# Optimization experiments

Hardware: AMD Instinct MI355X
Metric: run time of the kernel (lower is better)

Reference implementation:

```python
import jax, jax.numpy as jnp
import numpy as np

SCALE = 8.0  # (dim // n_heads) ** 0.5 = (1024 // 16) ** 0.5


def setup_inputs() -> dict:
    key = jax.random.key(0)
    kq, kk, kv = jax.random.split(key, 3)
    shape = (2, 16, 2048, 64)  # [B, H, N, Dh]
    q = jax.random.normal(kq, shape, dtype=jnp.float32)
    k = jax.random.normal(kk, shape, dtype=jnp.float32)
    v = jax.random.normal(kv, shape, dtype=jnp.float32)
    return {"q": q, "k": k, "v": v}


def reference(q, k, v):
    # scores[b,h,n,m] = sum_d q[b,h,n,d] * k[b,h,m,d], then MULTIPLIED by scale
    # (the original multiplies by sqrt(head_dim), it does not divide).
    scores = jnp.einsum('bhnd,bhmd->bhnm', q, k) * SCALE
    scores = jax.nn.softmax(scores, axis=-1)
    # Faithful to the original quirky einsum: sums over n (query axis), keeps m.
    # out[b,h,m,d] = (sum_n scores[b,h,n,m]) * v[b,h,m,d]
    out = jnp.einsum('bhnm,bhmd->bhmd', scores, v)
    return out
```

## Files before the change

### kernel.cpp

```cpp
#include <hip/hip_runtime.h>
#include <math.h>

#define BH 32
#define NN 2048
#define DD 64
#define BHNN (BH * NN)
#define QK ((size_t)BH * NN * DD)
#define LDK 72

#define QSCALE 11.5415603f

typedef __attribute__((ext_vector_type(8)))  _Float16 halfx8;
typedef __attribute__((ext_vector_type(4)))  _Float16 halfx4;
typedef __attribute__((ext_vector_type(16))) float    floatx16;

__device__ inline float fexp2(float x) { return __builtin_amdgcn_exp2f(x); }

__device__ inline int rowmap(int r, int half) {
    return (r & 3) + 8 * (r >> 2) + 4 * half;
}

__global__ __launch_bounds__(256) void convert_kernel(const float4* __restrict__ q,
                                                      const float4* __restrict__ k,
                                                      _Float16* __restrict__ qhi,
                                                      _Float16* __restrict__ qlo,
                                                      _Float16* __restrict__ khi) {
    size_t gid = (size_t)blockIdx.x * 256 + threadIdx.x;
    float4 qa = q[gid];
    float4 ka = k[gid];
    float qf[4] = {qa.x, qa.y, qa.z, qa.w};
    float kf[4] = {ka.x, ka.y, ka.z, ka.w};
    halfx4 h, l, kh;
#pragma unroll
    for (int i = 0; i < 4; ++i) {
        float f = qf[i] * QSCALE;
        _Float16 hh = (_Float16)f;
        h[i] = hh;
        l[i] = (_Float16)(f - (float)hh);
        kh[i] = (_Float16)kf[i];
    }
    *(halfx4*)&qhi[gid * 4] = h;
    *(halfx4*)&qlo[gid * 4] = l;
    *(halfx4*)&khi[gid * 4] = kh;
}

__device__ inline void load_tile(const _Float16* __restrict__ khi_t,
                                 int tid, halfx8 rh[4]) {
#pragma unroll
    for (int i = 0; i < 4; ++i) {
        int c = tid + 256 * i;
        int r = c >> 3, s = c & 7;
        rh[i] = *(const halfx8*)&khi_t[(size_t)r * 64 + s * 8];
    }
}
__device__ inline void write_tile(_Float16* Khi, int tid, const halfx8 rh[4]) {
#pragma unroll
    for (int i = 0; i < 4; ++i) {
        int c = tid + 256 * i;
        int r = c >> 3, s = c & 7;
        *(halfx8*)&Khi[r * LDK + s * 8] = rh[i];
    }
}

__device__ inline void load_a(const _Float16* __restrict__ qhi_row,
                              const _Float16* __restrict__ qlo_row,
                              int half, halfx8 ah[4], halfx8 al[4]) {
#pragma unroll
    for (int ks = 0; ks < 4; ++ks) {
        ah[ks] = *(const halfx8*)&qhi_row[ks * 16 + half * 8];
        al[ks] = *(const halfx8*)&qlo_row[ks * 16 + half * 8];
    }
}

__global__ __launch_bounds__(256, 3) void stats_kernel(const _Float16* __restrict__ qhi,
                                                       const _Float16* __restrict__ qlo,
                                                       const _Float16* __restrict__ khi,
                                                       float* __restrict__ smax_p,
                                                       float* __restrict__ sden_p) {
    __shared__ _Float16 Khi[128 * LDK];
    const int g    = blockIdx.x & 63;
    const int bh   = g & 31;
    const int ms   = g >> 5;
    const int n0   = (blockIdx.x >> 6) * 128;
    const int tid  = threadIdx.x;
    const int wave = tid >> 6, lane = tid & 63;
    const int half = lane >> 5, l31 = lane & 31;
    const size_t base = (size_t)bh * NN * DD;

    halfx8 ah[4], al[4];
    {
        size_t ro = base + (size_t)(n0 + wave * 32 + l31) * DD;
        load_a(qhi + ro, qlo + ro, half, ah, al);
    }

    float m_run[16], d_run[16];
#pragma unroll
    for (int r = 0; r < 16; ++r) { m_run[r] = -INFINITY; d_run[r] = 0.f; }

    const _Float16* khi_b = khi + base;
    halfx8 rh[4];
    load_tile(khi_b + (size_t)(ms * 8) * 8192, tid, rh);

    for (int mti = 0; mti < 8; ++mti) {
        __syncthreads();
        write_tile(Khi, tid, rh);
        __syncthreads();
        if (mti < 7) {
            size_t toff = (size_t)(ms * 8 + mti + 1) * 8192;
            load_tile(khi_b + toff, tid, rh);
        }

        floatx16 acc[4];
#pragma unroll
        for (int t = 0; t < 4; ++t)
#pragma unroll
            for (int e = 0; e < 16; ++e) acc[t][e] = 0.f;

#pragma unroll
        for (int t = 0; t < 4; ++t) {
            const int mr = t * 32 + l31;
#pragma unroll
            for (int ks = 0; ks < 4; ++ks) {
                halfx8 bhf = *(const halfx8*)&Khi[mr * LDK + ks * 16 + half * 8];
                acc[t] = __builtin_amdgcn_mfma_f32_32x32x16_f16(ah[ks], bhf, acc[t], 0, 0, 0);
                acc[t] = __builtin_amdgcn_mfma_f32_32x32x16_f16(al[ks], bhf, acc[t], 0, 0, 0);
            }
        }

#pragma unroll
        for (int r = 0; r < 16; ++r) {
            float tmax = fmaxf(fmaxf(acc[0][r], acc[1][r]), fmaxf(acc[2][r], acc[3][r]));
            float m_new = fmaxf(m_run[r], tmax);
            float s = fexp2(acc[0][r] - m_new) + fexp2(acc[1][r] - m_new)
                    + fexp2(acc[2][r] - m_new) + fexp2(acc[3][r] - m_new);
            d_run[r] = d_run[r] * fexp2(m_run[r] - m_new) + s;
            m_run[r] = m_new;
        }
    }

    float* smp = smax_p + ((size_t)ms * BH + bh) * NN;
    float* sdp = sden_p + ((size_t)ms * BH + bh) * NN;
#pragma unroll
    for (int r = 0; r < 16; ++r) {
        float M = m_run[r];
#pragma unroll
        for (int off = 1; off < 32; off <<= 1)
            M = fmaxf(M, __shfl_xor(M, off));
        float dd = d_run[r] * fexp2(m_run[r] - M);
#pragma unroll
        for (int off = 1; off < 32; off <<= 1)
            dd += __shfl_xor(dd, off);
        if (l31 == 0) {
            int row = n0 + wave * 32 + rowmap(r, half);
            smp[row] = M;
            sdp[row] = dd;
        }
    }
}

__global__ __launch_bounds__(256, 3) void wsum_kernel(const _Float16* __restrict__ qhi,
                                                      const _Float16* __restrict__ qlo,
                                                      const _Float16* __restrict__ khi,
                                                      const float* __restrict__ smax_p,
                                                      const float* __restrict__ sden_p,
                                                      float* __restrict__ wpart) {
    __shared__ _Float16 Khi[128 * LDK];
    __shared__ float wred[4 * 128];
    __shared__ float Ms[1024];
    __shared__ float Is[1024];
    const int g    = blockIdx.x & 63;
    const int bh   = g & 31;
    const int nz   = g >> 5;
    const int m0   = (blockIdx.x >> 6) * 128;
    const int tid  = threadIdx.x;
    const int wave = tid >> 6, lane = tid & 63;
    const int half = lane >> 5, l31 = lane & 31;
    const size_t base = (size_t)bh * NN * DD;

    {
        halfx8 rh[4];
        load_tile(khi + base + (size_t)m0 * 64, tid, rh);
        write_tile(Khi, tid, rh);
        size_t roff = (size_t)bh * NN + nz * 1024 + tid * 4;
        float4 m0v = *(const float4*)&smax_p[roff];
        float4 m1v = *(const float4*)&smax_p[(size_t)BHNN + roff];
        float4 d0v = *(const float4*)&sden_p[roff];
        float4 d1v = *(const float4*)&sden_p[(size_t)BHNN + roff];
        float mm0[4] = {m0v.x, m0v.y, m0v.z, m0v.w};
        float mm1[4] = {m1v.x, m1v.y, m1v.z, m1v.w};
        float dd0[4] = {d0v.x, d0v.y, d0v.z, d0v.w};
        float dd1[4] = {d1v.x, d1v.y, d1v.z, d1v.w};
#pragma unroll
        for (int j = 0; j < 4; ++j) {
            float M = fmaxf(mm0[j], mm1[j]);
            float den = dd0[j] * fexp2(mm0[j] - M) + dd1[j] * fexp2(mm1[j] - M);
            Ms[tid * 4 + j] = M;
            Is[tid * 4 + j] = 1.0f / den;
        }
    }
    __syncthreads();

    float wacc[4] = {0.f, 0.f, 0.f, 0.f};

#pragma unroll
    for (int it = 0; it < 8; ++it) {
        const int ls = wave + it * 4;
        halfx8 ah[4], al[4];
        {
            size_t ro = base + (size_t)((nz * 32 + ls) * 32 + l31) * DD;
            load_a(qhi + ro, qlo + ro, half, ah, al);
        }

        floatx16 acc[4];
#pragma unroll
        for (int t = 0; t < 4; ++t)
#pragma unroll
            for (int e = 0; e < 16; ++e) acc[t][e] = 0.f;

#pragma unroll
        for (int t = 0; t < 4; ++t) {
            const int mr = t * 32 + l31;
#pragma unroll
            for (int ks = 0; ks < 4; ++ks) {
                halfx8 bhf = *(const halfx8*)&Khi[mr * LDK + ks * 16 + half * 8];
                acc[t] = __builtin_amdgcn_mfma_f32_32x32x16_f16(ah[ks], bhf, acc[t], 0, 0, 0);
                acc[t] = __builtin_amdgcn_mfma_f32_32x32x16_f16(al[ks], bhf, acc[t], 0, 0, 0);
            }
        }

#pragma unroll
        for (int r = 0; r < 16; ++r) {
            const int lrow = ls * 32 + rowmap(r, half);
            float M   = Ms[lrow];
            float inv = Is[lrow];
#pragma unroll
            for (int t = 0; t < 4; ++t)
                wacc[t] += fexp2(acc[t][r] - M) * inv;
        }
    }

#pragma unroll
    for (int t = 0; t < 4; ++t) wacc[t] += __shfl_xor(wacc[t], 32);
    if (half == 0) {
#pragma unroll
        for (int t = 0; t < 4; ++t) wred[wave * 128 + t * 32 + l31] = wacc[t];
    }
    __syncthreads();
    if (tid < 128) {
        float s = wred[tid] + wred[128 + tid] + wred[256 + tid] + wred[384 + tid];
        wpart[((size_t)nz * BH + bh) * NN + m0 + tid] = s;
    }
}

__global__ __launch_bounds__(256) void out_kernel(const float* __restrict__ v,
                                                  const float* __restrict__ w0,
                                                  const float* __restrict__ w1,
                                                  float* __restrict__ out) {
    size_t gid = (size_t)blockIdx.x * 256 + threadIdx.x;
    const float4* v4 = (const float4*)v;
    float4* o4 = (float4*)out;
    float4 vv = v4[gid];
    float ww = w0[gid >> 4] + w1[gid >> 4];
    o4[gid] = make_float4(vv.x * ww, vv.y * ww, vv.z * ww, vv.w * ww);
}

extern "C" void kernel_launch(void* const* d_in, const int* in_sizes, int n_in,
                              void* d_out, int out_size, void* d_ws, size_t ws_size,
                              hipStream_t stream) {
    const float* q = (const float*)d_in[0];
    const float* k = (const float*)d_in[1];
    const float* v = (const float*)d_in[2];
    float* out = (float*)d_out;

    _Float16* qhi = (_Float16*)d_ws;
    _Float16* qlo = qhi + QK;
    _Float16* khi = qlo + QK;
    float* smax_p = (float*)(khi + QK);
    float* sden_p = smax_p + 2 * BHNN;
    float* wpart  = sden_p + 2 * BHNN;

    convert_kernel<<<QK / 4 / 256, 256, 0, stream>>>((const float4*)q, (const float4*)k,
                                                     qhi, qlo, khi);
    stats_kernel<<<1024, 256, 0, stream>>>(qhi, qlo, khi, smax_p, sden_p);
    wsum_kernel<<<1024, 256, 0, stream>>>(qhi, qlo, khi, smax_p, sden_p, wpart);
    out_kernel<<<(BH * NN * DD / 4) / 256, 256, 0, stream>>>(v, wpart, wpart + BHNN, out);
}
```

Baseline: 192.4 us.

## Stage K tiles via async global_load_lds with XOR-swizzled layout and double buffering

The convert kernel now writes the fp16 K copy in an XOR-swizzled order within each 64-element row. This lets the stats and wsum kernels copy K tiles straight from global memory into LDS with 16-byte global_load_lds, instead of staging them through registers, and without padding. The stats kernel double-buffers the K tile in LDS, so it needs one barrier per iteration instead of two, and the next tile's load overlaps the MFMA work. The risk is correctness if the swizzle or the async load's completion ordering is wrong; it also relies on the __syncthreads barrier to wait for the LDS DMA.

```diff
diff --git a/kernel.cpp b/kernel.cpp
--- a/kernel.cpp
+++ b/kernel.cpp
@@ -6,7 +6,6 @@
 #define DD 64
 #define BHNN (BH * NN)
 #define QK ((size_t)BH * NN * DD)
-#define LDK 72
 
 #define QSCALE 11.5415603f
 
@@ -41,24 +40,20 @@
     }
     *(halfx4*)&qhi[gid * 4] = h;
     *(halfx4*)&qlo[gid * 4] = l;
-    *(halfx4*)&khi[gid * 4] = kh;
-}
-
-__device__ inline void load_tile(const _Float16* __restrict__ khi_t,
-                                 int tid, halfx8 rh[4]) {
+    size_t rowbase = (gid * 4) & ~(size_t)63;
+    int j = (int)((gid >> 1) & 7) ^ (int)((gid >> 4) & 7);
+    *(halfx4*)&khi[rowbase + (size_t)(j << 3) + ((gid & 1) << 2)] = kh;
+}
+
+__device__ inline void stage_tile_async(const _Float16* __restrict__ gtile,
+                                        _Float16* lds, int wave, int lane) {
 #pragma unroll
     for (int i = 0; i < 4; ++i) {
-        int c = tid + 256 * i;
-        int r = c >> 3, s = c & 7;
-        rh[i] = *(const halfx8*)&khi_t[(size_t)r * 64 + s * 8];
-    }
-}
-__device__ inline void write_tile(_Float16* Khi, int tid, const halfx8 rh[4]) {
-#pragma unroll
-    for (int i = 0; i < 4; ++i) {
-        int c = tid + 256 * i;
-        int r = c >> 3, s = c & 7;
-        *(halfx8*)&Khi[r * LDK + s * 8] = rh[i];
+        const char* gp = (const char*)gtile + wave * 4096 + i * 1024 + lane * 16;
+        char* lp = (char*)lds + wave * 4096 + i * 1024;
+        __builtin_amdgcn_global_load_lds(
+            (const __attribute__((address_space(1))) unsigned int*)gp,
+            (__attribute__((address_space(3))) unsigned int*)lp, 16, 0, 0);
     }
 }
 
@@ -77,7 +72,7 @@
                                                        const _Float16* __restrict__ khi,
                                                        float* __restrict__ smax_p,
                                                        float* __restrict__ sden_p) {
-    __shared__ _Float16 Khi[128 * LDK];
+    __shared__ _Float16 K2[2 * 128 * 64];
     const int g    = blockIdx.x & 63;
     const int bh   = g & 31;
     const int ms   = g >> 5;
@@ -85,7 +80,11 @@
     const int tid  = threadIdx.x;
     const int wave = tid >> 6, lane = tid & 63;
     const int half = lane >> 5, l31 = lane & 31;
+    const int xr   = l31 & 7;
     const size_t base = (size_t)bh * NN * DD;
+
+    const _Float16* khi_b = khi + base;
+    stage_tile_async(khi_b + (size_t)(ms * 8) * 8192, K2, wave, lane);
 
     halfx8 ah[4], al[4];
     {
@@ -97,18 +96,13 @@
 #pragma unroll
     for (int r = 0; r < 16; ++r) { m_run[r] = -INFINITY; d_run[r] = 0.f; }
 
-    const _Float16* khi_b = khi + base;
-    halfx8 rh[4];
-    load_tile(khi_b + (size_t)(ms * 8) * 8192, tid, rh);
+    __syncthreads();
 
     for (int mti = 0; mti < 8; ++mti) {
-        __syncthreads();
-        write_tile(Khi, tid, rh);
-        __syncthreads();
-        if (mti < 7) {
-            size_t toff = (size_t)(ms * 8 + mti + 1) * 8192;
-            load_tile(khi_b + toff, tid, rh);
-        }
+        const _Float16* Kc = K2 + (mti & 1) * 8192;
+        if (mti < 7)
+            stage_tile_async(khi_b + (size_t)(ms * 8 + mti + 1) * 8192,
+                             K2 + ((mti + 1) & 1) * 8192, wave, lane);
 
         floatx16 acc[4];
 #pragma unroll
@@ -119,9 +113,11 @@
 #pragma unroll
         for (int t = 0; t < 4; ++t) {
             const int mr = t * 32 + l31;
+            const _Float16* rowp = Kc + (size_t)mr * 64;
 #pragma unroll
             for (int ks = 0; ks < 4; ++ks) {
-                halfx8 bhf = *(const halfx8*)&Khi[mr * LDK + ks * 16 + half * 8];
+                const int j = (ks * 2 + half) ^ xr;
+                halfx8 bhf = *(const halfx8*)&rowp[j << 3];
                 acc[t] = __builtin_amdgcn_mfma_f32_32x32x16_f16(ah[ks], bhf, acc[t], 0, 0, 0);
                 acc[t] = __builtin_amdgcn_mfma_f32_32x32x16_f16(al[ks], bhf, acc[t], 0, 0, 0);
             }
@@ -136,6 +132,8 @@
             d_run[r] = d_run[r] * fexp2(m_run[r] - m_new) + s;
             m_run[r] = m_new;
         }
+
+        if (mti < 7) __syncthreads();
     }
 
     float* smp = smax_p + ((size_t)ms * BH + bh) * NN;
@@ -164,7 +162,7 @@
                                                       const float* __restrict__ smax_p,
                                                       const float* __restrict__ sden_p,
                                                       float* __restrict__ wpart) {
-    __shared__ _Float16 Khi[128 * LDK];
+    __shared__ _Float16 Khi[128 * 64];
     __shared__ float wred[4 * 128];
     __shared__ float Ms[1024];
     __shared__ float Is[1024];
@@ -175,12 +173,12 @@
     const int tid  = threadIdx.x;
     const int wave = tid >> 6, lane = tid & 63;
     const int half = lane >> 5, l31 = lane & 31;
+    const int xr   = l31 & 7;
     const size_t base = (size_t)bh * NN * DD;
 
+    stage_tile_async(khi + base + (size_t)m0 * 64, Khi, wave, lane);
+
     {
-        halfx8 rh[4];
-        load_tile(khi + base + (size_t)m0 * 64, tid, rh);
-        write_tile(Khi, tid, rh);
         size_t roff = (size_t)bh * NN + nz * 1024 + tid * 4;
         float4 m0v = *(const float4*)&smax_p[roff];
         float4 m1v = *(const float4*)&smax_p[(size_t)BHNN + roff];
@@ -220,9 +218,11 @@
 #pragma unroll
         for (int t = 0; t < 4; ++t) {
             const int mr = t * 32 + l31;
+            const _Float16* rowp = Khi + (size_t)mr * 64;
 #pragma unroll
             for (int ks = 0; ks < 4; ++ks) {
-                halfx8 bhf = *(const halfx8*)&Khi[mr * LDK + ks * 16 + half * 8];
+                const int j = (ks * 2 + half) ^ xr;
+                halfx8 bhf = *(const halfx8*)&rowp[j << 3];
                 acc[t] = __builtin_amdgcn_mfma_f32_32x32x16_f16(ah[ks], bhf, acc[t], 0, 0, 0);
                 acc[t] = __builtin_amdgcn_mfma_f32_32x32x16_f16(al[ks], bhf, acc[t], 0, 0, 0);
             }
```

Result: no change. 192.5 us (+0.0%).
